# Optimization experiments

Measured on AMD Instinct MI355X. Metric: run time of the kernel, lower is better.

## Reference

```python
import jax, jax.numpy as jnp
import numpy as np

N = 50000
E = 800000
IN_DIM, HID_DIM, OUT_DIM = 128, 64, 32


def setup_inputs() -> dict:
    key = jax.random.key(0)
    k1, k2, k3, k4 = jax.random.split(key, 4)
    x = jax.random.normal(k1, (N, IN_DIM), dtype=jnp.float32)
    edge_index = jax.random.randint(k2, (2, E), 0, N, dtype=jnp.int64)
    # Glorot-style init for GCNConv weights, zero bias (PyG default)
    W1 = jax.random.normal(k3, (IN_DIM, HID_DIM), dtype=jnp.float32) / np.sqrt(IN_DIM)
    b1 = jnp.zeros((HID_DIM,), dtype=jnp.float32)
    W2 = jax.random.normal(k4, (HID_DIM, OUT_DIM), dtype=jnp.float32) / np.sqrt(HID_DIM)
    b2 = jnp.zeros((OUT_DIM,), dtype=jnp.float32)
    return {"x": x, "edge_index": edge_index, "W1": W1, "b1": b1, "W2": W2, "b2": b2}


def _gcn_norm(edge_index, num_nodes):
    # Add self-loops (PyG GCNConv default add_self_loops=True)
    loops = jnp.arange(num_nodes, dtype=edge_index.dtype)
    row = jnp.concatenate([edge_index[0], loops])  # source
    col = jnp.concatenate([edge_index[1], loops])  # target
    deg = jax.ops.segment_sum(jnp.ones_like(col, dtype=jnp.float32), col,
                              num_segments=num_nodes)
    dis = jnp.where(deg > 0, jax.lax.rsqrt(jnp.maximum(deg, 1.0)), 0.0)
    norm = dis[row] * dis[col]  # [E+N]
    return row, col, norm


def _gcn_conv(h, row, col, norm, W, b, num_nodes):
    h = h @ W                                   # [N, out]
    msg = h[row] * norm[:, None]                # gather + scale, [E+N, out]
    out = jax.ops.segment_sum(msg, col, num_segments=num_nodes)
    return out + b


def reference(x, edge_index, W1, b1, W2, b2):
    num_nodes = x.shape[0]
    row, col, norm = _gcn_norm(edge_index, num_nodes)
    h = _gcn_conv(x, row, col, norm, W1, b1, num_nodes)
    h = jax.nn.relu(h)
    out = _gcn_conv(h, row, col, norm, W2, b2, num_nodes)
    return out
```

## Files before the change

### kernel.cpp

```cpp
#include <hip/hip_runtime.h>
#include <hip/hip_fp16.h>

#define Nn    50000
#define Ee    800000
#define IND   128
#define HIDD  64
#define OUTD  32
#define NBUCK ((Nn + 255) / 256)
#define EPB   4096
#define NBB   ((Ee + EPB - 1) / EPB)
#define SCAP  6144
#define RB    64
#define GB    ((Nn + RB - 1) / RB)
#define XSTR  136

typedef _Float16 f16x8 __attribute__((ext_vector_type(8)));
typedef float    f32x4 __attribute__((ext_vector_type(4)));

__device__ __forceinline__ int ld_nt_i32(const int* p) {
    return __builtin_nontemporal_load(p);
}
__device__ __forceinline__ long long ld_nt_i64(const long long* p) {
    return __builtin_nontemporal_load(p);
}

__global__ __launch_bounds__(256) void k_bin(const void* __restrict__ p,
        int* __restrict__ gcur, unsigned int* __restrict__ staged) {
    __shared__ int hist[256], offs[256], lcur[256], gposs[256];
    __shared__ unsigned int stage[EPB];
    __shared__ unsigned int red[256];
    int t = threadIdx.x;
    int base0 = blockIdx.x * EPB;
    red[t] = ((const unsigned int*)p)[2 * (base0 + t) + 1];
    hist[t] = 0;
    __syncthreads();
    for (int s = 128; s > 0; s >>= 1) {
        if (t < s) red[t] |= red[t + s];
        __syncthreads();
    }
    bool f64 = (red[0] == 0u);
    int nv = Ee - base0; if (nv > EPB) nv = EPB;
    unsigned int pl[16];
    #pragma unroll
    for (int q = 0; q < 16; ++q) {
        int e = base0 + q * 256 + t;
        if (e < Ee) {
            int r, c;
            if (f64) { r = (int)ld_nt_i64((const long long*)p + e);
                       c = (int)ld_nt_i64((const long long*)p + Ee + e); }
            else     { r = ld_nt_i32((const int*)p + e);
                       c = ld_nt_i32((const int*)p + Ee + e); }
            pl[q] = ((unsigned int)c << 16) | (unsigned int)r;
            atomicAdd(&hist[pl[q] >> 24], 1);
        }
    }
    __syncthreads();
    int v = hist[t];
    offs[t] = v;
    __syncthreads();
    for (int off = 1; off < 256; off <<= 1) {
        int add = (t >= off) ? offs[t - off] : 0;
        __syncthreads();
        offs[t] += add;
        __syncthreads();
    }
    int excl = offs[t] - v;
    __syncthreads();
    offs[t] = excl;
    lcur[t] = excl;
    __syncthreads();
    #pragma unroll
    for (int q = 0; q < 16; ++q) {
        int e = base0 + q * 256 + t;
        if (e < Ee) {
            int bk = pl[q] >> 24;
            int pos = atomicAdd(&lcur[bk], 1);
            stage[pos] = pl[q];
        }
    }
    if (t < NBUCK) {
        int h = hist[t];
        gposs[t] = h ? atomicAdd(&gcur[t], h) : 0;
    }
    __syncthreads();
    for (int i = t; i < nv; i += 256) {
        unsigned int pv = stage[i];
        int bk = pv >> 24;
        int idx = gposs[bk] + (i - offs[bk]);
        if (idx < SCAP) staged[(size_t)bk * SCAP + idx] = pv;
    }
}

__global__ __launch_bounds__(256) void k_bsort(const unsigned int* __restrict__ staged,
        const int* __restrict__ gcur, int* __restrict__ rowstart,
        float* __restrict__ dis, unsigned short* __restrict__ slots) {
    __shared__ int bsc[256];
    __shared__ int hist[256], nodestart[256], cur[256];
    __shared__ unsigned short sortbuf[SCAP];
    int t = threadIdx.x, b = blockIdx.x;
    int gv = (t < NBUCK) ? min(gcur[t], SCAP) : 0;
    bsc[t] = gv;
    hist[t] = 0;
    __syncthreads();
    for (int off = 1; off < 256; off <<= 1) {
        int add = (t >= off) ? bsc[t - off] : 0;
        __syncthreads();
        bsc[t] += add;
        __syncthreads();
    }
    int bucketbase = (b == 0) ? 0 : bsc[b - 1];
    int m = bsc[b] - bucketbase;
    const unsigned int* sp = staged + (size_t)b * SCAP;
    for (int i = t; i < m; i += 256) atomicAdd(&hist[(sp[i] >> 16) & 255], 1);
    __syncthreads();
    int v = hist[t];
    nodestart[t] = v;
    __syncthreads();
    for (int off = 1; off < 256; off <<= 1) {
        int add = (t >= off) ? nodestart[t - off] : 0;
        __syncthreads();
        nodestart[t] += add;
        __syncthreads();
    }
    int excl = nodestart[t] - v;
    __syncthreads();
    nodestart[t] = excl;
    cur[t] = 0;
    int node = b * 256 + t;
    if (node < Nn) {
        rowstart[node] = bucketbase + excl;
        dis[node] = rsqrtf((float)v + 1.0f);
    }
    if (b == NBUCK - 1 && t == 0) rowstart[Nn] = Ee;
    __syncthreads();
    for (int i = t; i < m; i += 256) {
        unsigned int pv = sp[i];
        int lc = (pv >> 16) & 255;
        int pos = nodestart[lc] + atomicAdd(&cur[lc], 1);
        sortbuf[pos] = (unsigned short)(pv & 0xFFFFu);
    }
    __syncthreads();
    for (int i = t; i < m; i += 256) slots[bucketbase + i] = sortbuf[i];
}

__global__ __launch_bounds__(256) void k_gemm1(const float* __restrict__ x,
                                               const float* __restrict__ W,
                                               const float* __restrict__ dis,
                                               __half* __restrict__ h) {
    __shared__ _Float16 Xl[RB * XSTR];
    __shared__ _Float16 Wl[HIDD * XSTR];
    int t = threadIdx.x;
    int row0 = blockIdx.x * RB;
    for (int i = t; i < IND * HIDD; i += 256) {
        int k = i & 127, n = i >> 7;
        Wl[n * XSTR + k] = (_Float16)W[k * HIDD + n];
    }
    for (int i = t; i < RB * (IND / 4); i += 256) {
        int rr = i >> 5, kk = (i & 31) * 4;
        int gr = row0 + rr;
        float4 v = make_float4(0.f, 0.f, 0.f, 0.f);
        if (gr < Nn) v = ((const float4*)x)[(size_t)gr * (IND / 4) + (i & 31)];
        _Float16* dst = &Xl[rr * XSTR + kk];
        dst[0] = (_Float16)v.x; dst[1] = (_Float16)v.y;
        dst[2] = (_Float16)v.z; dst[3] = (_Float16)v.w;
    }
    __syncthreads();
    int wv = t >> 6, lane = t & 63;
    int m = lane & 15, quad = lane >> 4;
    f32x4 acc[4] = {{0.f,0.f,0.f,0.f},{0.f,0.f,0.f,0.f},
                    {0.f,0.f,0.f,0.f},{0.f,0.f,0.f,0.f}};
    const _Float16* xrow = &Xl[(wv * 16 + m) * XSTR + quad * 8];
    #pragma unroll
    for (int kt = 0; kt < 4; ++kt) {
        f16x8 av = *(const f16x8*)(xrow + kt * 32);
        #pragma unroll
        for (int ct = 0; ct < 4; ++ct) {
            f16x8 bv = *(const f16x8*)&Wl[(ct * 16 + m) * XSTR + kt * 32 + quad * 8];
            acc[ct] = __builtin_amdgcn_mfma_f32_16x16x32_f16(av, bv, acc[ct], 0, 0, 0);
        }
    }
    int rbase = row0 + wv * 16 + quad * 4;
    #pragma unroll
    for (int reg = 0; reg < 4; ++reg) {
        int gr = rbase + reg;
        if (gr < Nn) {
            float d = dis[gr];
            #pragma unroll
            for (int ct = 0; ct < 4; ++ct)
                h[(size_t)gr * HIDD + ct * 16 + m] = __float2half(d * acc[ct][reg]);
        }
    }
}

__global__ __launch_bounds__(256) void k_agg1(const unsigned short* __restrict__ slots,
        const int* __restrict__ rowstart, const float* __restrict__ dis,
        const __half2* __restrict__ h1, const float* __restrict__ b1,
        const float* __restrict__ W2, __half* __restrict__ h2) {
    __shared__ float sh[8][HIDD];
    __shared__ float W2s[HIDD * OUTD];
    int t = threadIdx.x;
    for (int i = t; i < HIDD * OUTD; i += 256) W2s[i] = W2[i];
    int sub = t >> 5, lane = t & 31;
    int n = blockIdx.x * 8 + sub;
    int s = rowstart[n], e = rowstart[n + 1];
    float d = dis[n];
    float2 acc = make_float2(0.f, 0.f);
    int p = s;
    while (p + 16 <= e) {
        int rv[16];
        #pragma unroll
        for (int q = 0; q < 16; ++q) rv[q] = slots[p + q];
        float2 fv[16];
        #pragma unroll
        for (int q = 0; q < 16; ++q) fv[q] = __half22float2(h1[rv[q] * 32 + lane]);
        #pragma unroll
        for (int q = 0; q < 16; ++q) { acc.x += fv[q].x; acc.y += fv[q].y; }
        p += 16;
    }
    if (p + 8 <= e) {
        int rv[8];
        #pragma unroll
        for (int q = 0; q < 8; ++q) rv[q] = slots[p + q];
        float2 fv[8];
        #pragma unroll
        for (int q = 0; q < 8; ++q) fv[q] = __half22float2(h1[rv[q] * 32 + lane]);
        #pragma unroll
        for (int q = 0; q < 8; ++q) { acc.x += fv[q].x; acc.y += fv[q].y; }
        p += 8;
    }
    for (; p < e; ++p) {
        float2 v = __half22float2(h1[(int)slots[p] * 32 + lane]);
        acc.x += v.x; acc.y += v.y;
    }
    float2 self = __half22float2(h1[n * 32 + lane]);
    float vx = b1[2 * lane]     + d * (acc.x + self.x);
    float vy = b1[2 * lane + 1] + d * (acc.y + self.y);
    sh[sub][2 * lane]     = fmaxf(vx, 0.0f);
    sh[sub][2 * lane + 1] = fmaxf(vy, 0.0f);
    __syncthreads();
    int jn = t >> 5, j = t & 31;
    float o = 0.0f;
    #pragma unroll
    for (int k = 0; k < HIDD; ++k) o = fmaf(sh[jn][k], W2s[k * OUTD + j], o);
    h2[(size_t)n * OUTD + j] = __float2half(d * o);
}

__global__ __launch_bounds__(256) void k_agg2(const unsigned short* __restrict__ slots,
        const int* __restrict__ rowstart, const float* __restrict__ dis,
        const __half2* __restrict__ h2, const float* __restrict__ b2,
        float* __restrict__ out) {
    int t = threadIdx.x;
    int sub = t >> 4, lane = t & 15;
    int n = blockIdx.x * 16 + sub;
    int s = rowstart[n], e = rowstart[n + 1];
    float d = dis[n];
    float2 acc = make_float2(0.f, 0.f);
    int p = s;
    while (p + 16 <= e) {
        int rv[16];
        #pragma unroll
        for (int q = 0; q < 16; ++q) rv[q] = slots[p + q];
        float2 fv[16];
        #pragma unroll
        for (int q = 0; q < 16; ++q) fv[q] = __half22float2(h2[rv[q] * 16 + lane]);
        #pragma unroll
        for (int q = 0; q < 16; ++q) { acc.x += fv[q].x; acc.y += fv[q].y; }
        p += 16;
    }
    if (p + 8 <= e) {
        int rv[8];
        #pragma unroll
        for (int q = 0; q < 8; ++q) rv[q] = slots[p + q];
        float2 fv[8];
        #pragma unroll
        for (int q = 0; q < 8; ++q) fv[q] = __half22float2(h2[rv[q] * 16 + lane]);
        #pragma unroll
        for (int q = 0; q < 8; ++q) { acc.x += fv[q].x; acc.y += fv[q].y; }
        p += 8;
    }
    for (; p < e; ++p) {
        float2 v = __half22float2(h2[(int)slots[p] * 16 + lane]);
        acc.x += v.x; acc.y += v.y;
    }
    float2 self = __half22float2(h2[n * 16 + lane]);
    float2 res;
    res.x = b2[2 * lane]     + d * (acc.x + self.x);
    res.y = b2[2 * lane + 1] + d * (acc.y + self.y);
    ((float2*)out)[n * 16 + lane] = res;
}

extern "C" void kernel_launch(void* const* d_in, const int* in_sizes, int n_in,
                              void* d_out, int out_size, void* d_ws, size_t ws_size,
                              hipStream_t stream) {
    const float* x  = (const float*)d_in[0];
    const void*  ei = d_in[1];
    const float* W1 = (const float*)d_in[2];
    const float* b1 = (const float*)d_in[3];
    const float* W2 = (const float*)d_in[4];
    const float* b2 = (const float*)d_in[5];
    float* out = (float*)d_out;

    char* w = (char*)d_ws;
    int*            gcur     = (int*)w;            w += ((size_t)NBUCK * 4 + 255) / 256 * 256;
    int*            rowstart = (int*)w;            w += (size_t)(Nn + 1) * 4 + 188;
    float*          dis      = (float*)w;          w += (size_t)Nn * 4;
    unsigned int*   staged   = (unsigned int*)w;   w += (size_t)NBUCK * SCAP * 4;
    unsigned short* slots    = (unsigned short*)w; w += (size_t)Ee * 2;
    __half*         h1       = (__half*)w;         w += (size_t)Nn * HIDD * 2;
    __half*         h2       = (__half*)w;         w += (size_t)Nn * OUTD * 2;

    hipMemsetAsync(gcur, 0, (size_t)NBUCK * 4, stream);
    k_bin  <<<NBB, 256, 0, stream>>>(ei, gcur, staged);
    k_bsort<<<NBUCK, 256, 0, stream>>>(staged, gcur, rowstart, dis, slots);
    k_gemm1<<<GB, 256, 0, stream>>>(x, W1, dis, h1);
    k_agg1 <<<Nn / 8, 256, 0, stream>>>(slots, rowstart, dis, (const __half2*)h1, b1, W2, h2);
    k_agg2 <<<Nn / 16, 256, 0, stream>>>(slots, rowstart, dis, (const __half2*)h2, b2, out);
}
```

Measured before the change: 177.7 us.

## Fuse edge binning with first GEMM and defer degree scaling to bucket sort

```diff
diff --git a/kernel.cpp b/kernel.cpp
--- a/kernel.cpp
+++ b/kernel.cpp
@@ -24,137 +24,94 @@
     return __builtin_nontemporal_load(p);
 }
 
-__global__ __launch_bounds__(256) void k_bin(const void* __restrict__ p,
-        int* __restrict__ gcur, unsigned int* __restrict__ staged) {
-    __shared__ int hist[256], offs[256], lcur[256], gposs[256];
-    __shared__ unsigned int stage[EPB];
-    __shared__ unsigned int red[256];
+__global__ void k_prep(const float* __restrict__ W, int* __restrict__ gcur,
+                       _Float16* __restrict__ WTg) {
     int t = threadIdx.x;
-    int base0 = blockIdx.x * EPB;
-    red[t] = ((const unsigned int*)p)[2 * (base0 + t) + 1];
-    hist[t] = 0;
-    __syncthreads();
-    for (int s = 128; s > 0; s >>= 1) {
-        if (t < s) red[t] |= red[t + s];
-        __syncthreads();
-    }
-    bool f64 = (red[0] == 0u);
-    int nv = Ee - base0; if (nv > EPB) nv = EPB;
-    unsigned int pl[16];
-    #pragma unroll
-    for (int q = 0; q < 16; ++q) {
-        int e = base0 + q * 256 + t;
-        if (e < Ee) {
-            int r, c;
-            if (f64) { r = (int)ld_nt_i64((const long long*)p + e);
-                       c = (int)ld_nt_i64((const long long*)p + Ee + e); }
-            else     { r = ld_nt_i32((const int*)p + e);
-                       c = ld_nt_i32((const int*)p + Ee + e); }
-            pl[q] = ((unsigned int)c << 16) | (unsigned int)r;
-            atomicAdd(&hist[pl[q] >> 24], 1);
-        }
-    }
-    __syncthreads();
-    int v = hist[t];
-    offs[t] = v;
-    __syncthreads();
-    for (int off = 1; off < 256; off <<= 1) {
-        int add = (t >= off) ? offs[t - off] : 0;
-        __syncthreads();
-        offs[t] += add;
-        __syncthreads();
-    }
-    int excl = offs[t] - v;
-    __syncthreads();
-    offs[t] = excl;
-    lcur[t] = excl;
-    __syncthreads();
-    #pragma unroll
-    for (int q = 0; q < 16; ++q) {
-        int e = base0 + q * 256 + t;
-        if (e < Ee) {
-            int bk = pl[q] >> 24;
-            int pos = atomicAdd(&lcur[bk], 1);
-            stage[pos] = pl[q];
-        }
-    }
-    if (t < NBUCK) {
-        int h = hist[t];
-        gposs[t] = h ? atomicAdd(&gcur[t], h) : 0;
-    }
-    __syncthreads();
-    for (int i = t; i < nv; i += 256) {
-        unsigned int pv = stage[i];
-        int bk = pv >> 24;
-        int idx = gposs[bk] + (i - offs[bk]);
-        if (idx < SCAP) staged[(size_t)bk * SCAP + idx] = pv;
-    }
-}
-
-__global__ __launch_bounds__(256) void k_bsort(const unsigned int* __restrict__ staged,
-        const int* __restrict__ gcur, int* __restrict__ rowstart,
-        float* __restrict__ dis, unsigned short* __restrict__ slots) {
-    __shared__ int bsc[256];
-    __shared__ int hist[256], nodestart[256], cur[256];
-    __shared__ unsigned short sortbuf[SCAP];
-    int t = threadIdx.x, b = blockIdx.x;
-    int gv = (t < NBUCK) ? min(gcur[t], SCAP) : 0;
-    bsc[t] = gv;
-    hist[t] = 0;
-    __syncthreads();
-    for (int off = 1; off < 256; off <<= 1) {
-        int add = (t >= off) ? bsc[t - off] : 0;
-        __syncthreads();
-        bsc[t] += add;
-        __syncthreads();
-    }
-    int bucketbase = (b == 0) ? 0 : bsc[b - 1];
-    int m = bsc[b] - bucketbase;
-    const unsigned int* sp = staged + (size_t)b * SCAP;
-    for (int i = t; i < m; i += 256) atomicAdd(&hist[(sp[i] >> 16) & 255], 1);
-    __syncthreads();
-    int v = hist[t];
-    nodestart[t] = v;
-    __syncthreads();
-    for (int off = 1; off < 256; off <<= 1) {
-        int add = (t >= off) ? nodestart[t - off] : 0;
-        __syncthreads();
-        nodestart[t] += add;
-        __syncthreads();
-    }
-    int excl = nodestart[t] - v;
-    __syncthreads();
-    nodestart[t] = excl;
-    cur[t] = 0;
-    int node = b * 256 + t;
-    if (node < Nn) {
-        rowstart[node] = bucketbase + excl;
-        dis[node] = rsqrtf((float)v + 1.0f);
-    }
-    if (b == NBUCK - 1 && t == 0) rowstart[Nn] = Ee;
-    __syncthreads();
-    for (int i = t; i < m; i += 256) {
-        unsigned int pv = sp[i];
-        int lc = (pv >> 16) & 255;
-        int pos = nodestart[lc] + atomicAdd(&cur[lc], 1);
-        sortbuf[pos] = (unsigned short)(pv & 0xFFFFu);
-    }
-    __syncthreads();
-    for (int i = t; i < m; i += 256) slots[bucketbase + i] = sortbuf[i];
-}
-
-__global__ __launch_bounds__(256) void k_gemm1(const float* __restrict__ x,
-                                               const float* __restrict__ W,
-                                               const float* __restrict__ dis,
-                                               __half* __restrict__ h) {
-    __shared__ _Float16 Xl[RB * XSTR];
-    __shared__ _Float16 Wl[HIDD * XSTR];
+    if (t < NBUCK) gcur[t] = 0;
+    for (int j = 0; j < 32; ++j) {
+        int idx = j * 256 + t;
+        int k = idx >> 6, n = idx & 63;
+        WTg[n * XSTR + k] = (_Float16)W[idx];
+    }
+}
+
+__global__ __launch_bounds__(256) void k_bin_gemm1(const void* __restrict__ p,
+        int* __restrict__ gcur, unsigned int* __restrict__ staged,
+        const float* __restrict__ x, const _Float16* __restrict__ WTg,
+        __half* __restrict__ h1raw) {
+    __shared__ alignas(16) char smem[21504];
     int t = threadIdx.x;
-    int row0 = blockIdx.x * RB;
-    for (int i = t; i < IND * HIDD; i += 256) {
-        int k = i & 127, n = i >> 7;
-        Wl[n * XSTR + k] = (_Float16)W[k * HIDD + n];
-    }
+    if (blockIdx.x < NBB) {
+        unsigned int* stage = (unsigned int*)smem;
+        int* hist  = (int*)(smem + 16384);
+        int* offs  = hist + 256;
+        int* lcur  = offs + 256;
+        int* gposs = lcur + 256;
+        unsigned int* red = (unsigned int*)(gposs + 256);
+        int base0 = blockIdx.x * EPB;
+        red[t] = ((const unsigned int*)p)[2 * (base0 + t) + 1];
+        hist[t] = 0;
+        __syncthreads();
+        for (int s = 128; s > 0; s >>= 1) {
+            if (t < s) red[t] |= red[t + s];
+            __syncthreads();
+        }
+        bool f64 = (red[0] == 0u);
+        int nv = Ee - base0; if (nv > EPB) nv = EPB;
+        unsigned int pl[16];
+        #pragma unroll
+        for (int q = 0; q < 16; ++q) {
+            int e = base0 + q * 256 + t;
+            if (e < Ee) {
+                int r, c;
+                if (f64) { r = (int)ld_nt_i64((const long long*)p + e);
+                           c = (int)ld_nt_i64((const long long*)p + Ee + e); }
+                else     { r = ld_nt_i32((const int*)p + e);
+                           c = ld_nt_i32((const int*)p + Ee + e); }
+                pl[q] = ((unsigned int)c << 16) | (unsigned int)r;
+                atomicAdd(&hist[pl[q] >> 24], 1);
+            }
+        }
+        __syncthreads();
+        int v = hist[t];
+        offs[t] = v;
+        __syncthreads();
+        for (int off = 1; off < 256; off <<= 1) {
+            int add = (t >= off) ? offs[t - off] : 0;
+            __syncthreads();
+            offs[t] += add;
+            __syncthreads();
+        }
+        int excl = offs[t] - v;
+        __syncthreads();
+        offs[t] = excl;
+        lcur[t] = excl;
+        __syncthreads();
+        #pragma unroll
+        for (int q = 0; q < 16; ++q) {
+            int e = base0 + q * 256 + t;
+            if (e < Ee) {
+                int bk = pl[q] >> 24;
+                int pos = atomicAdd(&lcur[bk], 1);
+                stage[pos] = pl[q];
+            }
+        }
+        if (t < NBUCK) {
+            int hh = hist[t];
+            gposs[t] = hh ? atomicAdd(&gcur[t], hh) : 0;
+        }
+        __syncthreads();
+        for (int i = t; i < nv; i += 256) {
+            unsigned int pv = stage[i];
+            int bk = pv >> 24;
+            int idx = gposs[bk] + (i - offs[bk]);
+            if (idx < SCAP) staged[(size_t)bk * SCAP + idx] = pv;
+        }
+        return;
+    }
+    _Float16* Xl = (_Float16*)smem;
+    int bid = blockIdx.x - NBB;
+    int row0 = bid * RB;
     for (int i = t; i < RB * (IND / 4); i += 256) {
         int rr = i >> 5, kk = (i & 31) * 4;
         int gr = row0 + rr;
@@ -175,7 +132,7 @@
         f16x8 av = *(const f16x8*)(xrow + kt * 32);
         #pragma unroll
         for (int ct = 0; ct < 4; ++ct) {
-            f16x8 bv = *(const f16x8*)&Wl[(ct * 16 + m) * XSTR + kt * 32 + quad * 8];
+            f16x8 bv = *(const f16x8*)&WTg[(ct * 16 + m) * XSTR + kt * 32 + quad * 8];
             acc[ct] = __builtin_amdgcn_mfma_f32_16x16x32_f16(av, bv, acc[ct], 0, 0, 0);
         }
     }
@@ -184,10 +141,74 @@
     for (int reg = 0; reg < 4; ++reg) {
         int gr = rbase + reg;
         if (gr < Nn) {
-            float d = dis[gr];
             #pragma unroll
             for (int ct = 0; ct < 4; ++ct)
-                h[(size_t)gr * HIDD + ct * 16 + m] = __float2half(d * acc[ct][reg]);
+                h1raw[(size_t)gr * HIDD + ct * 16 + m] = __float2half(acc[ct][reg]);
+        }
+    }
+}
+
+__global__ __launch_bounds__(256) void k_bsort(const unsigned int* __restrict__ staged,
+        const int* __restrict__ gcur, int* __restrict__ rowstart,
+        float* __restrict__ dis, unsigned short* __restrict__ slots,
+        __half2* __restrict__ h1v) {
+    __shared__ int bsc[256];
+    __shared__ int hist[256], nodestart[256], cur[256];
+    __shared__ float ndis[256];
+    __shared__ unsigned short sortbuf[SCAP];
+    int t = threadIdx.x, b = blockIdx.x;
+    int gv = (t < NBUCK) ? min(gcur[t], SCAP) : 0;
+    bsc[t] = gv;
+    hist[t] = 0;
+    __syncthreads();
+    for (int off = 1; off < 256; off <<= 1) {
+        int add = (t >= off) ? bsc[t - off] : 0;
+        __syncthreads();
+        bsc[t] += add;
+        __syncthreads();
+    }
+    int bucketbase = (b == 0) ? 0 : bsc[b - 1];
+    int m = bsc[b] - bucketbase;
+    const unsigned int* sp = staged + (size_t)b * SCAP;
+    for (int i = t; i < m; i += 256) atomicAdd(&hist[(sp[i] >> 16) & 255], 1);
+    __syncthreads();
+    int v = hist[t];
+    nodestart[t] = v;
+    __syncthreads();
+    for (int off = 1; off < 256; off <<= 1) {
+        int add = (t >= off) ? nodestart[t - off] : 0;
+        __syncthreads();
+        nodestart[t] += add;
+        __syncthreads();
+    }
+    int excl = nodestart[t] - v;
+    __syncthreads();
+    nodestart[t] = excl;
+    cur[t] = 0;
+    int node = b * 256 + t;
+    float dd = rsqrtf((float)v + 1.0f);
+    ndis[t] = dd;
+    if (node < Nn) {
+        rowstart[node] = bucketbase + excl;
+        dis[node] = dd;
+    }
+    if (b == NBUCK - 1 && t == 0) rowstart[Nn] = Ee;
+    __syncthreads();
+    for (int i = t; i < m; i += 256) {
+        unsigned int pv = sp[i];
+        int lc = (pv >> 16) & 255;
+        int pos = nodestart[lc] + atomicAdd(&cur[lc], 1);
+        sortbuf[pos] = (unsigned short)(pv & 0xFFFFu);
+    }
+    __syncthreads();
+    for (int i = t; i < m; i += 256) slots[bucketbase + i] = sortbuf[i];
+    for (int i = t; i < 256 * 32; i += 256) {
+        int nl = i >> 5;
+        int n = b * 256 + nl;
+        if (n < Nn) {
+            float2 f = __half22float2(h1v[(size_t)n * 32 + (i & 31)]);
+            float d = ndis[nl];
+            h1v[(size_t)n * 32 + (i & 31)] = __floats2half2_rn(d * f.x, d * f.y);
         }
     }
 }
@@ -304,15 +325,18 @@
     int*            gcur     = (int*)w;            w += ((size_t)NBUCK * 4 + 255) / 256 * 256;
     int*            rowstart = (int*)w;            w += (size_t)(Nn + 1) * 4 + 188;
     float*          dis      = (float*)w;          w += (size_t)Nn * 4;
+    _Float16*       WTg      = (_Float16*)w;       w += 64 * XSTR * 2 + 128;
     unsigned int*   staged   = (unsigned int*)w;   w += (size_t)NBUCK * SCAP * 4;
     unsigned short* slots    = (unsigned short*)w; w += (size_t)Ee * 2;
     __half*         h1       = (__half*)w;         w += (size_t)Nn * HIDD * 2;
     __half*         h2       = (__half*)w;         w += (size_t)Nn * OUTD * 2;
 
-    hipMemsetAsync(gcur, 0, (size_t)NBUCK * 4, stream);
-    k_bin  <<<NBB, 256, 0, stream>>>(ei, gcur, staged);
-    k_bsort<<<NBUCK, 256, 0, stream>>>(staged, gcur, rowstart, dis, slots);
-    k_gemm1<<<GB, 256, 0, stream>>>(x, W1, dis, h1);
-    k_agg1 <<<Nn / 8, 256, 0, stream>>>(slots, rowstart, dis, (const __half2*)h1, b1, W2, h2);
-    k_agg2 <<<Nn / 16, 256, 0, stream>>>(slots, rowstart, dis, (const __half2*)h2, b2, out);
-}
+    k_prep     <<<1, 256, 0, stream>>>(W1, gcur, WTg);
+    k_bin_gemm1<<<NBB + GB, 256, 0, stream>>>(ei, gcur, staged, x, WTg, h1);
+    k_bsort    <<<NBUCK, 256, 0, stream>>>(staged, gcur, rowstart, dis, slots,
+                                           (__half2*)h1);
+    k_agg1     <<<Nn / 8, 256, 0, stream>>>(slots, rowstart, dis, (const __half2*)h1,
+                                            b1, W2, h2);
+    k_agg2     <<<Nn / 16, 256, 0, stream>>>(slots, rowstart, dis, (const __half2*)h2,
+                                             b2, out);
+}
```

Result: faster. 172.2 us (-3.1%).
